# Kernel optimization log

Measured on AMD Instinct MI355X. Metric: run time of the kernel, lower is better.

## Reference

```python
import jax, jax.numpy as jnp
import numpy as np

C_IN = 256
C_INTER = C_IN // 2  # max(1, C//2)
B, D, H, W = 2, 16, 64, 64


def setup_inputs() -> dict:
    key = jax.random.key(0)
    ks = jax.random.split(key, 9)
    s = 1.0 / np.sqrt(C_IN)
    si = 1.0 / np.sqrt(C_INTER)
    return {
        "x": jax.random.normal(ks[0], (B, C_IN, D, H, W), dtype=jnp.float32),
        # 1x1x1 conv weights reduce to [out, in] matrices
        "g_w": jax.random.normal(ks[1], (C_INTER, C_IN), dtype=jnp.float32) * s,
        "g_b": jax.random.normal(ks[2], (C_INTER,), dtype=jnp.float32) * s,
        "theta_w": jax.random.normal(ks[3], (C_INTER, C_IN), dtype=jnp.float32) * s,
        "theta_b": jax.random.normal(ks[4], (C_INTER,), dtype=jnp.float32) * s,
        "phi_w": jax.random.normal(ks[5], (C_INTER, C_IN), dtype=jnp.float32) * s,
        "phi_b": jax.random.normal(ks[6], (C_INTER,), dtype=jnp.float32) * s,
        # note: torch code inits W to zero; random here so gradients/outputs are non-trivial
        "W_w": jax.random.normal(ks[7], (C_IN, C_INTER), dtype=jnp.float32) * si,
        "W_b": jax.random.normal(ks[8], (C_IN,), dtype=jnp.float32) * si,
    }


def reference(x, g_w, g_b, theta_w, theta_b, phi_w, phi_b, W_w, W_b):
    b, c, d, h, w = x.shape
    n = d * h * w
    xf = x.reshape(b, c, n)  # [B, C, N]
    # 1x1x1 convs == per-position linear projections
    g = jnp.einsum('oc,bcn->bon', g_w, xf) + g_b[None, :, None]        # [B, Ci, N]
    th = jnp.einsum('oc,bcn->bon', theta_w, xf) + theta_b[None, :, None]
    ph = jnp.einsum('oc,bcn->bon', phi_w, xf) + phi_b[None, :, None]
    # f = theta^T @ phi (N x N), y = (f / N) @ g^T. Since the normalizer is a
    # constant, reassociate: kv = phi @ g^T is [Ci, Ci], avoiding the NxN matrix.
    kv = jnp.einsum('bin,bjn->bij', ph, g)                              # [B, Ci, Ci]
    y = jnp.einsum('bin,bij->bjn', th, kv) / n                          # [B, Ci, N]
    y = jnp.einsum('oc,bcn->bon', W_w, y) + W_b[None, :, None]          # [B, C, N]
    return x + y.reshape(b, c, d, h, w)
```

## Files before the change

### kernel.cpp

```cpp
#include <hip/hip_runtime.h>

#define NB 2
#define CC 256
#define CI 128
#define NN 65536
#define LDA 72
#define LDX 264

typedef __bf16 bf16x8 __attribute__((ext_vector_type(8)));
typedef float f32x4 __attribute__((ext_vector_type(4)));

__device__ __forceinline__ unsigned short f2bf(float f) {
  unsigned u = __float_as_uint(f);
  u += 0x7fffu + ((u >> 16) & 1u);
  return (unsigned short)(u >> 16);
}

__global__ __launch_bounds__(512) void nl3d_syrk2(const float* __restrict__ x,
                                                  float* __restrict__ S,
                                                  float* __restrict__ partials,
                                                  float* __restrict__ svec,
                                                  int kchunk, int use_partial) {
  __shared__ unsigned short lds[256 * LDA];
  const int tid = threadIdx.x;
  const int lane = tid & 63;
  const int wv = tid >> 6;
  const int wm = wv & 3, wn = wv >> 2;
  const int b = blockIdx.y;
  const int kc0 = blockIdx.x * kchunk;

  const float* xb = x + (size_t)b * CC * NN;
  f32x4 acc[4][8];
  const f32x4 zero4 = {0.f, 0.f, 0.f, 0.f};
#pragma unroll
  for (int i = 0; i < 4; ++i)
#pragma unroll
    for (int j = 0; j < 8; ++j) acc[i][j] = zero4;

  float rsum[8];
#pragma unroll
  for (int i = 0; i < 8; ++i) rsum[i] = 0.f;

  const int r0 = tid >> 4;
  const int c4 = tid & 15;

  const int stages = kchunk >> 6;
  for (int s = 0; s < stages; ++s) {
    const int kc = kc0 + s * 64;
    float4 f[8];
#pragma unroll
    for (int i = 0; i < 8; ++i) {
      int row = r0 + 32 * i;
      f[i] = *(const float4*)(xb + (size_t)row * NN + kc + c4 * 4);
    }
    __syncthreads();
#pragma unroll
    for (int i = 0; i < 8; ++i) {
      int row = r0 + 32 * i;
      ushort4 h;
      h.x = f2bf(f[i].x); h.y = f2bf(f[i].y); h.z = f2bf(f[i].z); h.w = f2bf(f[i].w);
      *(ushort4*)&lds[row * LDA + c4 * 4] = h;
      rsum[i] += f[i].x + f[i].y + f[i].z + f[i].w;
    }
    __syncthreads();

    const int m = lane & 15;
    const int kg = (lane >> 4) * 8;
#pragma unroll
    for (int kk = 0; kk < 2; ++kk) {
      bf16x8 afr[4], bfr[8];
#pragma unroll
      for (int mt = 0; mt < 4; ++mt)
        afr[mt] = *(const bf16x8*)&lds[(wm * 64 + mt * 16 + m) * LDA + kk * 32 + kg];
#pragma unroll
      for (int nt = 0; nt < 8; ++nt)
        bfr[nt] = *(const bf16x8*)&lds[(wn * 128 + nt * 16 + m) * LDA + kk * 32 + kg];
#pragma unroll
      for (int mt = 0; mt < 4; ++mt)
#pragma unroll
        for (int nt = 0; nt < 8; ++nt)
          acc[mt][nt] = __builtin_amdgcn_mfma_f32_16x16x32_bf16(afr[mt], bfr[nt], acc[mt][nt], 0, 0, 0);
    }
  }

  const int col = lane & 15;
  const int rq = (lane >> 4) * 4;
  if (use_partial) {
    float* dst = partials + ((size_t)(b * gridDim.x + blockIdx.x)) * (CC * CC);
#pragma unroll
    for (int mt = 0; mt < 4; ++mt)
#pragma unroll
      for (int nt = 0; nt < 8; ++nt)
#pragma unroll
        for (int r = 0; r < 4; ++r) {
          int gi = wm * 64 + mt * 16 + rq + r;
          int gj = wn * 128 + nt * 16 + col;
          dst[gi * CC + gj] = acc[mt][nt][r];
        }
  } else {
    float* Sb = S + (size_t)b * CC * CC;
#pragma unroll
    for (int mt = 0; mt < 4; ++mt)
#pragma unroll
      for (int nt = 0; nt < 8; ++nt)
#pragma unroll
        for (int r = 0; r < 4; ++r) {
          int gi = wm * 64 + mt * 16 + rq + r;
          int gj = wn * 128 + nt * 16 + col;
          atomicAdd(&Sb[gi * CC + gj], acc[mt][nt][r]);
        }
  }

  __syncthreads();
  float* ldsRS = (float*)lds;
  if (tid < 256) ldsRS[tid] = 0.f;
  __syncthreads();
#pragma unroll
  for (int i = 0; i < 8; ++i) atomicAdd(&ldsRS[r0 + 32 * i], rsum[i]);
  __syncthreads();
  if (tid < 256) atomicAdd(&svec[b * CC + tid], ldsRS[tid]);
}

__global__ __launch_bounds__(256) void nl3d_reduce(const float* __restrict__ partials,
                                                   float* __restrict__ S, int splits) {
  const int e = blockIdx.x * 256 + threadIdx.x;
  const int b = e >> 14;
  const int off = e & 16383;
  const float4* p = (const float4*)partials;
  float4 a0 = {0, 0, 0, 0}, a1 = {0, 0, 0, 0};
  const size_t base = (size_t)b * splits * 16384 + off;
  for (int s = 0; s < splits; s += 2) {
    float4 v0 = p[base + (size_t)s * 16384];
    float4 v1 = p[base + (size_t)(s + 1) * 16384];
    a0.x += v0.x; a0.y += v0.y; a0.z += v0.z; a0.w += v0.w;
    a1.x += v1.x; a1.y += v1.y; a1.z += v1.z; a1.w += v1.w;
  }
  float4 r;
  r.x = a0.x + a1.x; r.y = a0.y + a1.y; r.z = a0.z + a1.z; r.w = a0.w + a1.w;
  ((float4*)S)[e] = r;
}

__global__ void nl3d_b0(const float* __restrict__ g_w, float* __restrict__ gwT) {
  int t = blockIdx.x * 256 + threadIdx.x;
  int j = t >> 8, d = t & 255;
  gwT[d * CI + j] = g_w[t];
}

__global__ void nl3d_b1(const float* __restrict__ phi_w, const float* __restrict__ S,
                        float* __restrict__ P) {
  int b = blockIdx.x >> 7, i = blockIdx.x & 127, d = threadIdx.x;
  const float* Sb = S + (size_t)b * CC * CC;
  const float* ph = phi_w + i * CC;
  float a0 = 0.f, a1 = 0.f, a2 = 0.f, a3 = 0.f;
  for (int c = 0; c < CC; c += 4) {
    a0 += ph[c + 0] * Sb[(c + 0) * CC + d];
    a1 += ph[c + 1] * Sb[(c + 1) * CC + d];
    a2 += ph[c + 2] * Sb[(c + 2) * CC + d];
    a3 += ph[c + 3] * Sb[(c + 3) * CC + d];
  }
  P[((size_t)b * CI + i) * CC + d] = (a0 + a1) + (a2 + a3);
}

__global__ void nl3d_b2(const float* __restrict__ P, const float* __restrict__ gwT,
                        const float* __restrict__ svec, const float* __restrict__ phi_w,
                        const float* __restrict__ phi_b, const float* __restrict__ g_b,
                        float* __restrict__ kv) {
  int b = blockIdx.x >> 7, i = blockIdx.x & 127, j = threadIdx.x;
  const float* Pr = P + ((size_t)b * CI + i) * CC;
  const float* sv = svec + b * CC;
  const float* ph = phi_w + i * CC;
  float u0 = 0.f, u1 = 0.f;
  for (int c = 0; c < CC; c += 2) {
    u0 += ph[c] * sv[c];
    u1 += ph[c + 1] * sv[c + 1];
  }
  float a0 = 0.f, a1 = 0.f, v0 = 0.f, v1 = 0.f;
  for (int d = 0; d < CC; d += 2) {
    float gT0 = gwT[d * CI + j], gT1 = gwT[(d + 1) * CI + j];
    a0 += Pr[d] * gT0; a1 += Pr[d + 1] * gT1;
    v0 += sv[d] * gT0; v1 += sv[d + 1] * gT1;
  }
  kv[((size_t)b * CI + i) * CI + j] =
      (a0 + a1) + (u0 + u1) * g_b[j] + phi_b[i] * ((v0 + v1) + (float)NN * g_b[j]);
}

__global__ void nl3d_b3(const float* __restrict__ kv, const float* __restrict__ theta_w,
                        const float* __restrict__ theta_b, float* __restrict__ T2,
                        float* __restrict__ tb2) {
  int b = blockIdx.x >> 7, j = blockIdx.x & 127, c = threadIdx.x;
  const float* kvb = kv + (size_t)b * CI * CI;
  float a0 = 0.f, a1 = 0.f;
  for (int i = 0; i < CI; i += 2) {
    a0 += kvb[i * CI + j] * theta_w[i * CC + c];
    a1 += kvb[(i + 1) * CI + j] * theta_w[(i + 1) * CC + c];
  }
  T2[((size_t)b * CI + j) * CC + c] = a0 + a1;
  if (c == 0) {
    float t = 0.f;
    for (int i = 0; i < CI; ++i) t += kvb[i * CI + j] * theta_b[i];
    tb2[b * CI + j] = t;
  }
}

__global__ void nl3d_b4(const float* __restrict__ T2, const float* __restrict__ tb2,
                        const float* __restrict__ W_w, const float* __restrict__ W_b,
                        unsigned short* __restrict__ Mbf, float* __restrict__ cvec) {
  int b = blockIdx.x >> 8, o = blockIdx.x & 255, c = threadIdx.x;
  const float inv = 1.0f / (float)NN;
  const float* Wr = W_w + o * CI;
  float a0 = 0.f, a1 = 0.f;
  for (int j = 0; j < CI; j += 2) {
    a0 += Wr[j] * T2[((size_t)b * CI + j) * CC + c];
    a1 += Wr[j + 1] * T2[((size_t)b * CI + j + 1) * CC + c];
  }
  Mbf[((size_t)b * CC + o) * CC + c] = f2bf((a0 + a1) * inv);
  if (c == 0) {
    float t = 0.f;
    for (int j = 0; j < CI; ++j) t += Wr[j] * tb2[b * CI + j];
    cvec[b * CC + o] = t * inv + W_b[o];
  }
}

__global__ __launch_bounds__(256) void nl3d_out(const float* __restrict__ x,
                                                const unsigned short* __restrict__ Mbf,
                                                const float* __restrict__ cvec,
                                                float* __restrict__ out) {
  __shared__ unsigned short xT[64 * LDX];
  const int tid = threadIdx.x;
  const int lane = tid & 63;
  const int wv = tid >> 6;
  const int b = blockIdx.y;
  const int n0 = blockIdx.x * 64;

  const float* xb = x + (size_t)b * CC * NN;
  float* ob = out + (size_t)b * CC * NN;

  {
    const int c4 = tid & 15;
#pragma unroll
    for (int i = 0; i < 8; ++i) {
      int p = i * 16 + (tid >> 4);
      float4 f0 = *(const float4*)(xb + (size_t)(2 * p) * NN + n0 + c4 * 4);
      float4 f1 = *(const float4*)(xb + (size_t)(2 * p + 1) * NN + n0 + c4 * 4);
      float a0[4] = {f0.x, f0.y, f0.z, f0.w};
      float a1[4] = {f1.x, f1.y, f1.z, f1.w};
      int ps = p ^ ((c4 & 7) << 2);
#pragma unroll
      for (int j = 0; j < 4; ++j) {
        unsigned pack = (unsigned)f2bf(a0[j]) | ((unsigned)f2bf(a1[j]) << 16);
        *(unsigned*)&xT[(c4 * 4 + j) * LDX + 2 * ps] = pack;
      }
    }
  }
  __syncthreads();

  f32x4 acc[4][4];
  const f32x4 zero4 = {0.f, 0.f, 0.f, 0.f};
#pragma unroll
  for (int i = 0; i < 4; ++i)
#pragma unroll
    for (int j = 0; j < 4; ++j) acc[i][j] = zero4;

  const int m = lane & 15;
  const int kg = (lane >> 4) * 8;
  const unsigned short* Mb = Mbf + (size_t)b * CC * CC;
#pragma unroll
  for (int kc = 0; kc < 8; ++kc) {
    bf16x8 afr[4], bfr[4];
#pragma unroll
    for (int mt = 0; mt < 4; ++mt)
      afr[mt] = *(const bf16x8*)(Mb + (size_t)(wv * 64 + mt * 16 + m) * CC + kc * 32 + kg);
#pragma unroll
    for (int nt = 0; nt < 4; ++nt) {
      int rr = nt * 16 + m;
      int d0 = (kc * 16 + (kg >> 1)) ^ (((rr >> 2) & 7) << 2);
      bfr[nt] = *(const bf16x8*)&xT[rr * LDX + 2 * d0];
    }
#pragma unroll
    for (int mt = 0; mt < 4; ++mt)
#pragma unroll
      for (int nt = 0; nt < 4; ++nt)
        acc[mt][nt] = __builtin_amdgcn_mfma_f32_16x16x32_bf16(afr[mt], bfr[nt], acc[mt][nt], 0, 0, 0);
  }

  const int col = lane & 15;
  const int rquad = (lane >> 4) * 4;
#pragma unroll
  for (int mt = 0; mt < 4; ++mt)
#pragma unroll
    for (int r = 0; r < 4; ++r) {
      int o = wv * 64 + mt * 16 + rquad + r;
      float cv = cvec[b * CC + o];
      const float* xrow = xb + (size_t)o * NN + n0;
      float* orow = ob + (size_t)o * NN + n0;
#pragma unroll
      for (int nt = 0; nt < 4; ++nt) {
        int n = nt * 16 + col;
        orow[n] = xrow[n] + acc[mt][nt][r] + cv;
      }
    }
}

extern "C" void kernel_launch(void* const* d_in, const int* in_sizes, int n_in,
                              void* d_out, int out_size, void* d_ws, size_t ws_size,
                              hipStream_t stream) {
  const float* x       = (const float*)d_in[0];
  const float* g_w     = (const float*)d_in[1];
  const float* g_b     = (const float*)d_in[2];
  const float* theta_w = (const float*)d_in[3];
  const float* theta_b = (const float*)d_in[4];
  const float* phi_w   = (const float*)d_in[5];
  const float* phi_b   = (const float*)d_in[6];
  const float* W_w     = (const float*)d_in[7];
  const float* W_b     = (const float*)d_in[8];
  float* out = (float*)d_out;

  char* ws = (char*)d_ws;
  float* S    = (float*)(ws);
  float* svec = (float*)(ws + 524288);
  float* P    = (float*)(ws + 526336);
  float* gwT  = (float*)(ws + 788480);
  float* kv   = (float*)(ws + 919552);
  float* T2   = (float*)(ws + 1050624);
  float* tb2  = (float*)(ws + 1312768);
  unsigned short* Mbf = (unsigned short*)(ws + 1313792);
  float* cvec = (float*)(ws + 1575936);
  float* partials = (float*)(ws + 2097152);

  int splits = 0;
  for (int c = 128; c >= 8; c >>= 1) {
    if (2097152 + (size_t)NB * c * CC * CC * 4 <= ws_size) { splits = c; break; }
  }

  if (splits > 0) {
    hipMemsetAsync(svec, 0, 2048, stream);
    nl3d_syrk2<<<dim3(splits, NB), 512, 0, stream>>>(x, S, partials, svec,
                                                     NN / splits, 1);
    nl3d_reduce<<<128, 256, 0, stream>>>(partials, S, splits);
  } else {
    hipMemsetAsync(ws, 0, 526336, stream);
    nl3d_syrk2<<<dim3(64, NB), 512, 0, stream>>>(x, S, (float*)ws, svec,
                                                 NN / 64, 0);
  }
  nl3d_b0<<<128, 256, 0, stream>>>(g_w, gwT);
  nl3d_b1<<<NB * CI, 256, 0, stream>>>(phi_w, S, P);
  nl3d_b2<<<NB * CI, 128, 0, stream>>>(P, gwT, svec, phi_w, phi_b, g_b, kv);
  nl3d_b3<<<NB * CI, 256, 0, stream>>>(kv, theta_w, theta_b, T2, tb2);
  nl3d_b4<<<NB * CC, 256, 0, stream>>>(T2, tb2, W_w, W_b, Mbf, cvec);
  nl3d_out<<<dim3(NN / 64, NB), 256, 0, stream>>>(x, Mbf, cvec, out);
}
```

Baseline: 395.7 us.

## Swap MFMA operands for vectorized float4 epilogues and prefetch A fragments

Swaps the A/B operands of the MFMA calls in both the Gram (syrk) and output kernels, so each lane's four accumulator values lie along contiguous columns. This lets the partial-sum writes and the residual epilogue use float4 loads and stores instead of scalar strided accesses. The output kernel also batches its x loads before converting them, prefetches the next k-chunk of M fragments from global memory, and sets a min-blocks-per-CU occupancy hint. The cost is more live registers, which may clash with the occupancy bound of 4.

```diff
diff --git a/kernel.cpp b/kernel.cpp
--- a/kernel.cpp
+++ b/kernel.cpp
@@ -79,7 +79,7 @@
       for (int mt = 0; mt < 4; ++mt)
 #pragma unroll
         for (int nt = 0; nt < 8; ++nt)
-          acc[mt][nt] = __builtin_amdgcn_mfma_f32_16x16x32_bf16(afr[mt], bfr[nt], acc[mt][nt], 0, 0, 0);
+          acc[mt][nt] = __builtin_amdgcn_mfma_f32_16x16x32_bf16(bfr[nt], afr[mt], acc[mt][nt], 0, 0, 0);
     }
   }
 
@@ -88,15 +88,17 @@
   if (use_partial) {
     float* dst = partials + ((size_t)(b * gridDim.x + blockIdx.x)) * (CC * CC);
 #pragma unroll
-    for (int mt = 0; mt < 4; ++mt)
-#pragma unroll
-      for (int nt = 0; nt < 8; ++nt)
-#pragma unroll
-        for (int r = 0; r < 4; ++r) {
-          int gi = wm * 64 + mt * 16 + rq + r;
-          int gj = wn * 128 + nt * 16 + col;
-          dst[gi * CC + gj] = acc[mt][nt][r];
-        }
+    for (int mt = 0; mt < 4; ++mt) {
+      const int gi = wm * 64 + mt * 16 + col;
+#pragma unroll
+      for (int nt = 0; nt < 8; ++nt) {
+        const int gj = wn * 128 + nt * 16 + rq;
+        float4 v;
+        v.x = acc[mt][nt][0]; v.y = acc[mt][nt][1];
+        v.z = acc[mt][nt][2]; v.w = acc[mt][nt][3];
+        *(float4*)&dst[(size_t)gi * CC + gj] = v;
+      }
+    }
   } else {
     float* Sb = S + (size_t)b * CC * CC;
 #pragma unroll
@@ -105,9 +107,9 @@
       for (int nt = 0; nt < 8; ++nt)
 #pragma unroll
         for (int r = 0; r < 4; ++r) {
-          int gi = wm * 64 + mt * 16 + rq + r;
-          int gj = wn * 128 + nt * 16 + col;
-          atomicAdd(&Sb[gi * CC + gj], acc[mt][nt][r]);
+          int gi = wm * 64 + mt * 16 + col;
+          int gj = wn * 128 + nt * 16 + rq + r;
+          atomicAdd(&Sb[(size_t)gi * CC + gj], acc[mt][nt][r]);
         }
   }
 
@@ -221,10 +223,10 @@
   }
 }
 
-__global__ __launch_bounds__(256) void nl3d_out(const float* __restrict__ x,
-                                                const unsigned short* __restrict__ Mbf,
-                                                const float* __restrict__ cvec,
-                                                float* __restrict__ out) {
+__global__ __launch_bounds__(256, 4) void nl3d_out(const float* __restrict__ x,
+                                                   const unsigned short* __restrict__ Mbf,
+                                                   const float* __restrict__ cvec,
+                                                   float* __restrict__ out) {
   __shared__ unsigned short xT[64 * LDX];
   const int tid = threadIdx.x;
   const int lane = tid & 63;
@@ -237,18 +239,27 @@
 
   {
     const int c4 = tid & 15;
-#pragma unroll
-    for (int i = 0; i < 8; ++i) {
-      int p = i * 16 + (tid >> 4);
-      float4 f0 = *(const float4*)(xb + (size_t)(2 * p) * NN + n0 + c4 * 4);
-      float4 f1 = *(const float4*)(xb + (size_t)(2 * p + 1) * NN + n0 + c4 * 4);
-      float a0[4] = {f0.x, f0.y, f0.z, f0.w};
-      float a1[4] = {f1.x, f1.y, f1.z, f1.w};
-      int ps = p ^ ((c4 & 7) << 2);
-#pragma unroll
-      for (int j = 0; j < 4; ++j) {
-        unsigned pack = (unsigned)f2bf(a0[j]) | ((unsigned)f2bf(a1[j]) << 16);
-        *(unsigned*)&xT[(c4 * 4 + j) * LDX + 2 * ps] = pack;
+    const int t4 = tid >> 4;
+#pragma unroll
+    for (int h = 0; h < 2; ++h) {
+      float4 f0[4], f1[4];
+#pragma unroll
+      for (int u = 0; u < 4; ++u) {
+        int p = (h * 4 + u) * 16 + t4;
+        f0[u] = *(const float4*)(xb + (size_t)(2 * p) * NN + n0 + c4 * 4);
+        f1[u] = *(const float4*)(xb + (size_t)(2 * p + 1) * NN + n0 + c4 * 4);
+      }
+#pragma unroll
+      for (int u = 0; u < 4; ++u) {
+        int p = (h * 4 + u) * 16 + t4;
+        int ps = p ^ ((c4 & 7) << 2);
+        float a0[4] = {f0[u].x, f0[u].y, f0[u].z, f0[u].w};
+        float a1[4] = {f1[u].x, f1[u].y, f1[u].z, f1[u].w};
+#pragma unroll
+        for (int j = 0; j < 4; ++j) {
+          unsigned pack = (unsigned)f2bf(a0[j]) | ((unsigned)f2bf(a1[j]) << 16);
+          *(unsigned*)&xT[(c4 * 4 + j) * LDX + 2 * ps] = pack;
+        }
       }
     }
   }
@@ -264,12 +275,22 @@
   const int m = lane & 15;
   const int kg = (lane >> 4) * 8;
   const unsigned short* Mb = Mbf + (size_t)b * CC * CC;
+
+  bf16x8 afr[4];
+#pragma unroll
+  for (int mt = 0; mt < 4; ++mt)
+    afr[mt] = *(const bf16x8*)(Mb + (size_t)(wv * 64 + mt * 16 + m) * CC + kg);
 #pragma unroll
   for (int kc = 0; kc < 8; ++kc) {
-    bf16x8 afr[4], bfr[4];
-#pragma unroll
-    for (int mt = 0; mt < 4; ++mt)
-      afr[mt] = *(const bf16x8*)(Mb + (size_t)(wv * 64 + mt * 16 + m) * CC + kc * 32 + kg);
+    bf16x8 cur[4];
+#pragma unroll
+    for (int mt = 0; mt < 4; ++mt) cur[mt] = afr[mt];
+    if (kc < 7) {
+#pragma unroll
+      for (int mt = 0; mt < 4; ++mt)
+        afr[mt] = *(const bf16x8*)(Mb + (size_t)(wv * 64 + mt * 16 + m) * CC + (kc + 1) * 32 + kg);
+    }
+    bf16x8 bfr[4];
 #pragma unroll
     for (int nt = 0; nt < 4; ++nt) {
       int rr = nt * 16 + m;
@@ -280,25 +301,31 @@
     for (int mt = 0; mt < 4; ++mt)
 #pragma unroll
       for (int nt = 0; nt < 4; ++nt)
-        acc[mt][nt] = __builtin_amdgcn_mfma_f32_16x16x32_bf16(afr[mt], bfr[nt], acc[mt][nt], 0, 0, 0);
-  }
-
-  const int col = lane & 15;
+        acc[mt][nt] = __builtin_amdgcn_mfma_f32_16x16x32_bf16(bfr[nt], cur[mt], acc[mt][nt], 0, 0, 0);
+  }
+
+  const int colo = lane & 15;
   const int rquad = (lane >> 4) * 4;
 #pragma unroll
-  for (int mt = 0; mt < 4; ++mt)
-#pragma unroll
-    for (int r = 0; r < 4; ++r) {
-      int o = wv * 64 + mt * 16 + rquad + r;
-      float cv = cvec[b * CC + o];
-      const float* xrow = xb + (size_t)o * NN + n0;
-      float* orow = ob + (size_t)o * NN + n0;
-#pragma unroll
-      for (int nt = 0; nt < 4; ++nt) {
-        int n = nt * 16 + col;
-        orow[n] = xrow[n] + acc[mt][nt][r] + cv;
-      }
-    }
+  for (int mt = 0; mt < 4; ++mt) {
+    const int o = wv * 64 + mt * 16 + colo;
+    const float cv = cvec[b * CC + o];
+    const float* xrow = xb + (size_t)o * NN + n0;
+    float* orow = ob + (size_t)o * NN + n0;
+    float4 xv[4];
+#pragma unroll
+    for (int nt = 0; nt < 4; ++nt)
+      xv[nt] = *(const float4*)(xrow + nt * 16 + rquad);
+#pragma unroll
+    for (int nt = 0; nt < 4; ++nt) {
+      float4 r;
+      r.x = xv[nt].x + acc[mt][nt][0] + cv;
+      r.y = xv[nt].y + acc[mt][nt][1] + cv;
+      r.z = xv[nt].z + acc[mt][nt][2] + cv;
+      r.w = xv[nt].w + acc[mt][nt][3] + cv;
+      *(float4*)(orow + nt * 16 + rquad) = r;
+    }
+  }
 }
 
 extern "C" void kernel_launch(void* const* d_in, const int* in_sizes, int n_in,
```

Result: slower. 419.5 us (+6.0%).

## Double-buffer LDS in Gram kernel and vectorize partial stores via swapped MFMA operands

Applied to the files above, without the earlier changes.

Splits LDS into two buffers and prefetches the next 64-column slab of x into registers while the MFMAs run on the current buffer, so there is one barrier per stage instead of two. MFMA operands are swapped so each lane holds four consecutive output columns, which lets the partial-sum epilogue write float4 instead of scalar stores. LDS use doubles (about 74KB) and prefetch registers are added, which may lower occupancy.

```diff
diff --git a/kernel.cpp b/kernel.cpp
--- a/kernel.cpp
+++ b/kernel.cpp
@@ -21,7 +21,7 @@
                                                   float* __restrict__ partials,
                                                   float* __restrict__ svec,
                                                   int kchunk, int use_partial) {
-  __shared__ unsigned short lds[256 * LDA];
+  __shared__ unsigned short lds[2][256 * LDA];
   const int tid = threadIdx.x;
   const int lane = tid & 63;
   const int wv = tid >> 6;
@@ -43,44 +43,68 @@
 
   const int r0 = tid >> 4;
   const int c4 = tid & 15;
+  const int m = lane & 15;
+  const int kg = (lane >> 4) * 8;
 
   const int stages = kchunk >> 6;
-  for (int s = 0; s < stages; ++s) {
-    const int kc = kc0 + s * 64;
+
+  {
     float4 f[8];
 #pragma unroll
-    for (int i = 0; i < 8; ++i) {
-      int row = r0 + 32 * i;
-      f[i] = *(const float4*)(xb + (size_t)row * NN + kc + c4 * 4);
-    }
-    __syncthreads();
+    for (int i = 0; i < 8; ++i)
+      f[i] = *(const float4*)(xb + (size_t)(r0 + 32 * i) * NN + kc0 + c4 * 4);
 #pragma unroll
     for (int i = 0; i < 8; ++i) {
       int row = r0 + 32 * i;
       ushort4 h;
       h.x = f2bf(f[i].x); h.y = f2bf(f[i].y); h.z = f2bf(f[i].z); h.w = f2bf(f[i].w);
-      *(ushort4*)&lds[row * LDA + c4 * 4] = h;
+      *(ushort4*)&lds[0][row * LDA + c4 * 4] = h;
       rsum[i] += f[i].x + f[i].y + f[i].z + f[i].w;
     }
-    __syncthreads();
-
-    const int m = lane & 15;
-    const int kg = (lane >> 4) * 8;
+  }
+  __syncthreads();
+
+  int cur = 0;
+  for (int s = 0; s < stages; ++s) {
+    float4 g[8];
+    const bool pf = (s + 1 < stages);
+    if (pf) {
+      const int kc = kc0 + (s + 1) * 64;
+#pragma unroll
+      for (int i = 0; i < 8; ++i)
+        g[i] = *(const float4*)(xb + (size_t)(r0 + 32 * i) * NN + kc + c4 * 4);
+    }
+
+    const unsigned short* L = lds[cur];
 #pragma unroll
     for (int kk = 0; kk < 2; ++kk) {
       bf16x8 afr[4], bfr[8];
 #pragma unroll
       for (int mt = 0; mt < 4; ++mt)
-        afr[mt] = *(const bf16x8*)&lds[(wm * 64 + mt * 16 + m) * LDA + kk * 32 + kg];
+        afr[mt] = *(const bf16x8*)&L[(wm * 64 + mt * 16 + m) * LDA + kk * 32 + kg];
 #pragma unroll
       for (int nt = 0; nt < 8; ++nt)
-        bfr[nt] = *(const bf16x8*)&lds[(wn * 128 + nt * 16 + m) * LDA + kk * 32 + kg];
+        bfr[nt] = *(const bf16x8*)&L[(wn * 128 + nt * 16 + m) * LDA + kk * 32 + kg];
 #pragma unroll
       for (int mt = 0; mt < 4; ++mt)
 #pragma unroll
         for (int nt = 0; nt < 8; ++nt)
-          acc[mt][nt] = __builtin_amdgcn_mfma_f32_16x16x32_bf16(afr[mt], bfr[nt], acc[mt][nt], 0, 0, 0);
-    }
+          acc[mt][nt] = __builtin_amdgcn_mfma_f32_16x16x32_bf16(bfr[nt], afr[mt], acc[mt][nt], 0, 0, 0);
+    }
+
+    if (pf) {
+      unsigned short* Lw = (unsigned short*)lds[cur ^ 1];
+#pragma unroll
+      for (int i = 0; i < 8; ++i) {
+        int row = r0 + 32 * i;
+        ushort4 h;
+        h.x = f2bf(g[i].x); h.y = f2bf(g[i].y); h.z = f2bf(g[i].z); h.w = f2bf(g[i].w);
+        *(ushort4*)&Lw[row * LDA + c4 * 4] = h;
+        rsum[i] += g[i].x + g[i].y + g[i].z + g[i].w;
+      }
+    }
+    __syncthreads();
+    cur ^= 1;
   }
 
   const int col = lane & 15;
@@ -88,15 +112,17 @@
   if (use_partial) {
     float* dst = partials + ((size_t)(b * gridDim.x + blockIdx.x)) * (CC * CC);
 #pragma unroll
-    for (int mt = 0; mt < 4; ++mt)
-#pragma unroll
-      for (int nt = 0; nt < 8; ++nt)
-#pragma unroll
-        for (int r = 0; r < 4; ++r) {
-          int gi = wm * 64 + mt * 16 + rq + r;
-          int gj = wn * 128 + nt * 16 + col;
-          dst[gi * CC + gj] = acc[mt][nt][r];
-        }
+    for (int mt = 0; mt < 4; ++mt) {
+      const int gi = wm * 64 + mt * 16 + col;
+#pragma unroll
+      for (int nt = 0; nt < 8; ++nt) {
+        const int gj = wn * 128 + nt * 16 + rq;
+        float4 v;
+        v.x = acc[mt][nt][0]; v.y = acc[mt][nt][1];
+        v.z = acc[mt][nt][2]; v.w = acc[mt][nt][3];
+        *(float4*)&dst[(size_t)gi * CC + gj] = v;
+      }
+    }
   } else {
     float* Sb = S + (size_t)b * CC * CC;
 #pragma unroll
@@ -105,14 +131,14 @@
       for (int nt = 0; nt < 8; ++nt)
 #pragma unroll
         for (int r = 0; r < 4; ++r) {
-          int gi = wm * 64 + mt * 16 + rq + r;
-          int gj = wn * 128 + nt * 16 + col;
-          atomicAdd(&Sb[gi * CC + gj], acc[mt][nt][r]);
+          int gi = wm * 64 + mt * 16 + col;
+          int gj = wn * 128 + nt * 16 + rq + r;
+          atomicAdd(&Sb[(size_t)gi * CC + gj], acc[mt][nt][r]);
         }
   }
 
   __syncthreads();
-  float* ldsRS = (float*)lds;
+  float* ldsRS = (float*)lds[0];
   if (tid < 256) ldsRS[tid] = 0.f;
   __syncthreads();
 #pragma unroll
```

New measurement: 400.7 us. Within noise of the previous version (+1.2%).
